# Kernel optimization log

Hardware: AMD Instinct MI355X
Metric: run time of the kernel (lower is better)

## Reference

```python
import jax, jax.numpy as jnp
import numpy as np

H = 1024      # hidden_size
I = 2 * H     # intermediate_size (expand_factor=2)
N = 16        # ssm_state_size
K = 4         # conv_kernel
BATCH = 2
SEQ = 2048


def setup_inputs() -> dict:
    key = jax.random.key(0)
    k = jax.random.split(key, 6)
    x = jax.random.normal(k[0], (BATCH, SEQ, H), dtype=jnp.float32)
    # nn.Linear default init ~ U(-1/sqrt(fan_in), 1/sqrt(fan_in)); scale is fine for a reference
    W_in = jax.random.normal(k[1], (2 * I, H), dtype=jnp.float32) / np.sqrt(H)
    conv_w = jax.random.normal(k[2], (I, 1, K), dtype=jnp.float32) / np.sqrt(K)
    W_x = jax.random.normal(k[3], (2 * N + 1, I), dtype=jnp.float32) / np.sqrt(I)
    A_log = jax.random.normal(k[4], (I, N), dtype=jnp.float32)
    D = jnp.ones((I,), dtype=jnp.float32)
    W_out = jax.random.normal(k[5], (H, I), dtype=jnp.float32) / np.sqrt(I)
    return {"x": x, "W_in": W_in, "conv_w": conv_w, "W_x": W_x,
            "A_log": A_log, "D": D, "W_out": W_out}


def reference(x, W_in, conv_w, W_x, A_log, D, W_out):
    xz = jnp.einsum('bsh,ih->bsi', x, W_in)
    xp, z = jnp.split(xz, 2, axis=-1)
    # depthwise causal conv1d: pad left K-1 (torch pads both sides then slices [:S])
    xc = jax.lax.conv_general_dilated(
        xp.transpose(0, 2, 1),           # (B, I, S)
        conv_w,                          # (I, 1, K) = OIH with groups=I
        window_strides=(1,),
        padding=[(K - 1, 0)],
        feature_group_count=I,
        dimension_numbers=('NCH', 'OIH', 'NCH'),
    ).transpose(0, 2, 1)                 # (B, S, I)
    xc = jax.nn.silu(xc)
    # x_proj -> delta (1), B (N), C (N)
    xproj = jnp.einsum('bsi,pi->bsp', xc, W_x)   # (B,S,2N+1)
    delta = jax.nn.softplus(xproj[..., :1])       # (B,S,1)
    Bmat = xproj[..., 1:1 + N]                    # (B,S,N)
    Cmat = xproj[..., 1 + N:]                     # (B,S,N)
    A = -jnp.exp(A_log)                           # (I,N)
    # decay/states broadcast-reduce: (B,S,I,N) intermediates reduced over N
    decay = jnp.exp(delta[..., None] * A[None, None])            # (B,S,I,N)
    states = xc[..., None] * Bmat[:, :, None, :] * decay          # (B,S,I,N)
    y = jnp.sum(states * Cmat[:, :, None, :], axis=-1)            # (B,S,I)
    y = y + xc * D[None, None, :]
    return jnp.einsum('bsi,hi->bsh', y * jax.nn.silu(z), W_out)
```

## Files before the change

### kernel.cpp

```cpp
#include <hip/hip_runtime.h>

#define LOG2E 1.4426950408889634f

__device__ __forceinline__ float b2f(unsigned short u) {
    unsigned int v = ((unsigned int)u) << 16;
    return __builtin_bit_cast(float, v);
}
__device__ __forceinline__ unsigned short f2b(float f) {
    unsigned int u = __builtin_bit_cast(unsigned int, f);
    u += 0x7fffu + ((u >> 16) & 1u);
    return (unsigned short)(u >> 16);
}
__device__ __forceinline__ float fexp(float x) {
    return __builtin_amdgcn_exp2f(x * LOG2E);
}
__device__ __forceinline__ float silu_f(float x) {
    return x * __builtin_amdgcn_rcpf(1.0f + fexp(-x));
}

typedef const __attribute__((address_space(1))) unsigned int* gas_t;
typedef __attribute__((address_space(3))) unsigned int* las_t;
__device__ __forceinline__ void gl2lds16(const unsigned short* g, unsigned short* l) {
    __builtin_amdgcn_global_load_lds((gas_t)(const void*)g, (las_t)(void*)l, 16, 0, 0);
}

__global__ __launch_bounds__(256) void cvt_all_k(const float* __restrict__ x,
                                                 const float* __restrict__ W_in,
                                                 const float* __restrict__ W_out,
                                                 const float* __restrict__ W_x,
                                                 unsigned short* __restrict__ xb,
                                                 unsigned short* __restrict__ wib,
                                                 unsigned short* __restrict__ wob,
                                                 unsigned short* __restrict__ wxb) {
    int b = blockIdx.x;
    const float* src;
    unsigned short* dst;
    if (b < 4096)       { src = x;     dst = xb;  }
    else if (b < 8192)  { src = W_in;  dst = wib; b -= 4096; }
    else if (b < 10240) { src = W_out; dst = wob; b -= 8192; }
    else                { src = W_x;   dst = wxb; b -= 10240; }
    int i = b * 256 + threadIdx.x;
    float4 v = ((const float4*)src)[i];
    *(ushort4*)(dst + (size_t)i * 4) = make_ushort4(f2b(v.x), f2b(v.y), f2b(v.z), f2b(v.w));
}

typedef __bf16 bf16x8 __attribute__((ext_vector_type(8)));
typedef float  fx4    __attribute__((ext_vector_type(4)));
typedef int    ix4    __attribute__((ext_vector_type(4)));
union FragU { ix4 i; bf16x8 b; };

template <bool OUT_BF16>
__global__ __launch_bounds__(256) void gemm_bt(const unsigned short* __restrict__ A,
                                               const unsigned short* __restrict__ B,
                                               void* __restrict__ C, int N, int K) {
    __shared__ __align__(16) unsigned short sA[128 * 64];
    __shared__ __align__(16) unsigned short sB[128 * 64];
    const int tid  = threadIdx.x;
    const int lane = tid & 63, wave = tid >> 6;
    const int bm = blockIdx.y * 128, bn = blockIdx.x * 128;
    const int wm = (wave >> 1) * 64, wn = (wave & 1) * 64;
    const int row16 = lane & 15, quad = lane >> 4;
    const int srow = lane >> 3;
    const int sc16 = (lane & 7) ^ srow;
    const unsigned short* gA = A + (size_t)(bm + wave * 32 + srow) * K + sc16 * 8;
    const unsigned short* gB = B + (size_t)(bn + wave * 32 + srow) * K + sc16 * 8;
    unsigned short* lA = sA + (wave * 4) * 512;
    unsigned short* lB = sB + (wave * 4) * 512;
    fx4 acc[4][4] = {};

    for (int kt = 0; kt < K; kt += 64) {
#pragma unroll
        for (int it = 0; it < 4; ++it) {
            gl2lds16(gA + (size_t)it * 8 * K + kt, lA + it * 512);
            gl2lds16(gB + (size_t)it * 8 * K + kt, lB + it * 512);
        }
        __syncthreads();
#pragma unroll
        for (int kk = 0; kk < 64; kk += 32) {
            FragU af[4], bf[4];
#pragma unroll
            for (int t = 0; t < 4; ++t) {
                int ra = wm + t * 16 + row16;
                af[t].i = *(const ix4*)(sA + ra * 64 + ((quad + (kk >> 3)) ^ (ra & 7)) * 8);
            }
#pragma unroll
            for (int t = 0; t < 4; ++t) {
                int rb = wn + t * 16 + row16;
                bf[t].i = *(const ix4*)(sB + rb * 64 + ((quad + (kk >> 3)) ^ (rb & 7)) * 8);
            }
#pragma unroll
            for (int tm = 0; tm < 4; ++tm)
#pragma unroll
                for (int tn = 0; tn < 4; ++tn)
                    acc[tm][tn] = __builtin_amdgcn_mfma_f32_16x16x32_bf16(
                        af[tm].b, bf[tn].b, acc[tm][tn], 0, 0, 0);
        }
        __syncthreads();
    }
#pragma unroll
    for (int tm = 0; tm < 4; ++tm) {
        int row0 = bm + wm + tm * 16 + quad * 4;
#pragma unroll
        for (int tn = 0; tn < 4; ++tn) {
            int col = bn + wn + tn * 16 + row16;
#pragma unroll
            for (int r = 0; r < 4; ++r) {
                float v = acc[tm][tn][r];
                if (OUT_BF16)
                    ((unsigned short*)C)[(size_t)(row0 + r) * N + col] = f2b(v);
                else
                    ((float*)C)[(size_t)(row0 + r) * N + col] = v;
            }
        }
    }
}

__global__ __launch_bounds__(256) void gemm_bt_n64(const unsigned short* __restrict__ A,
                                                   const unsigned short* __restrict__ B,
                                                   float* __restrict__ C, int N, int K) {
    __shared__ __align__(16) unsigned short sA[128 * 64];
    __shared__ __align__(16) unsigned short sB[64 * 64];
    const int tid  = threadIdx.x;
    const int lane = tid & 63, wave = tid >> 6;
    const int bm = blockIdx.y * 128, bn = blockIdx.x * 64;
    const int wm = wave * 32;
    const int row16 = lane & 15, quad = lane >> 4;
    const int srow = lane >> 3;
    const int sc16 = (lane & 7) ^ srow;
    const unsigned short* gA = A + (size_t)(bm + wave * 32 + srow) * K + sc16 * 8;
    const unsigned short* gB = B + (size_t)(bn + wave * 16 + srow) * K + sc16 * 8;
    unsigned short* lA = sA + (wave * 4) * 512;
    unsigned short* lB = sB + (wave * 2) * 512;
    fx4 acc[2][4] = {};

    for (int kt = 0; kt < K; kt += 64) {
#pragma unroll
        for (int it = 0; it < 4; ++it)
            gl2lds16(gA + (size_t)it * 8 * K + kt, lA + it * 512);
#pragma unroll
        for (int it = 0; it < 2; ++it)
            gl2lds16(gB + (size_t)it * 8 * K + kt, lB + it * 512);
        __syncthreads();
#pragma unroll
        for (int kk = 0; kk < 64; kk += 32) {
            FragU af[2], bf[4];
#pragma unroll
            for (int t = 0; t < 2; ++t) {
                int ra = wm + t * 16 + row16;
                af[t].i = *(const ix4*)(sA + ra * 64 + ((quad + (kk >> 3)) ^ (ra & 7)) * 8);
            }
#pragma unroll
            for (int t = 0; t < 4; ++t) {
                int rb = t * 16 + row16;
                bf[t].i = *(const ix4*)(sB + rb * 64 + ((quad + (kk >> 3)) ^ (rb & 7)) * 8);
            }
#pragma unroll
            for (int tm = 0; tm < 2; ++tm)
#pragma unroll
                for (int tn = 0; tn < 4; ++tn)
                    acc[tm][tn] = __builtin_amdgcn_mfma_f32_16x16x32_bf16(
                        af[tm].b, bf[tn].b, acc[tm][tn], 0, 0, 0);
        }
        __syncthreads();
    }
#pragma unroll
    for (int tm = 0; tm < 2; ++tm) {
        int row0 = bm + wm + tm * 16 + quad * 4;
#pragma unroll
        for (int tn = 0; tn < 4; ++tn) {
            int col = bn + tn * 16 + row16;
#pragma unroll
            for (int r = 0; r < 4; ++r)
                C[(size_t)(row0 + r) * N + col] = acc[tm][tn][r];
        }
    }
}

__global__ __launch_bounds__(256) void fused_mid_k(const unsigned short* __restrict__ xz,
                                                   const float* __restrict__ cw,
                                                   const unsigned short* __restrict__ wxb,
                                                   const float* __restrict__ Alog,
                                                   const float* __restrict__ Dv,
                                                   unsigned short* __restrict__ y2) {
    __shared__ __align__(16) unsigned short sxc[8 * 2048];
    __shared__ float sX[4][16][49];
    __shared__ float sdg[8 * 17];
    const int tid  = threadIdx.x;
    const int lane = tid & 63, wave = tid >> 6;
    const int row16 = lane & 15, quad = lane >> 4;
    const int m0 = blockIdx.x * 8;

    {
        const float4* cw4 = (const float4*)cw;
        float w[8][4];
#pragma unroll
        for (int c = 0; c < 8; ++c) {
            float4 t4 = cw4[tid * 8 + c];
            w[c][0] = t4.x; w[c][1] = t4.y; w[c][2] = t4.z; w[c][3] = t4.w;
        }
#pragma unroll
        for (int j = 0; j < 8; ++j) {
            const int m = m0 + j, s = m & 2047;
            float acc[8] = {0, 0, 0, 0, 0, 0, 0, 0};
#pragma unroll
            for (int k = 0; k < 4; ++k) {
                if (s - 3 + k >= 0) {
                    const unsigned short* p = xz + (size_t)(m - 3 + k) * 4096 + tid * 8;
                    ushort4 a = *(const ushort4*)p;
                    ushort4 b = *(const ushort4*)(p + 4);
                    float v[8] = {b2f(a.x), b2f(a.y), b2f(a.z), b2f(a.w),
                                  b2f(b.x), b2f(b.y), b2f(b.z), b2f(b.w)};
#pragma unroll
                    for (int c = 0; c < 8; ++c) acc[c] += v[c] * w[c][k];
                }
            }
            unsigned short* q = sxc + j * 2048 + ((tid ^ (j & 7)) * 8);
            *(ushort4*)q       = make_ushort4(f2b(silu_f(acc[0])), f2b(silu_f(acc[1])),
                                              f2b(silu_f(acc[2])), f2b(silu_f(acc[3])));
            *(ushort4*)(q + 4) = make_ushort4(f2b(silu_f(acc[4])), f2b(silu_f(acc[5])),
                                              f2b(silu_f(acc[6])), f2b(silu_f(acc[7])));
        }
    }
    __syncthreads();

    {
        fx4 acc[3] = {};
        const unsigned short* bp = wxb + (size_t)row16 * 2048 + wave * 512 + quad * 8;
        const int arow = row16 & 7;
        const int cbase = wave * 64 + quad;
#pragma unroll 4
        for (int kk = 0; kk < 512; kk += 32) {
            FragU a, b0, b1, b2;
            int c16 = cbase + (kk >> 3);
            a.i  = *(const ix4*)(sxc + arow * 2048 + ((c16 ^ (arow & 7)) * 8));
            b0.i = *(const ix4*)(bp + kk);
            b1.i = *(const ix4*)(bp + 16 * 2048 + kk);
            b2.i = *(const ix4*)(bp + 32 * 2048 + kk);
            acc[0] = __builtin_amdgcn_mfma_f32_16x16x32_bf16(a.b, b0.b, acc[0], 0, 0, 0);
            acc[1] = __builtin_amdgcn_mfma_f32_16x16x32_bf16(a.b, b1.b, acc[1], 0, 0, 0);
            acc[2] = __builtin_amdgcn_mfma_f32_16x16x32_bf16(a.b, b2.b, acc[2], 0, 0, 0);
        }
#pragma unroll
        for (int t = 0; t < 3; ++t)
#pragma unroll
            for (int r = 0; r < 4; ++r)
                sX[wave][quad * 4 + r][t * 16 + row16] = acc[t][r];
    }
    __syncthreads();
    for (int idx = tid; idx < 136; idx += 256) {
        int rr = idx / 17, q = idx - rr * 17;
        float o;
        if (q == 0) {
            float v = sX[0][rr][0] + sX[1][rr][0] + sX[2][rr][0] + sX[3][rr][0];
            o = (v > 20.f) ? v : log1pf(fexp(v));
        } else {
            float bs = sX[0][rr][q]      + sX[1][rr][q]      + sX[2][rr][q]      + sX[3][rr][q];
            float cs = sX[0][rr][q + 16] + sX[1][rr][q + 16] + sX[2][rr][q + 16] + sX[3][rr][q + 16];
            o = bs * cs;
        }
        sdg[rr * 17 + q] = o;
    }
    __syncthreads();

#pragma unroll 1
    for (int p = 0; p < 2; ++p) {
        const int ch0 = p * 1024 + tid * 4;
        float a2[4][16];
#pragma unroll
        for (int c = 0; c < 4; ++c) {
            const float4* ar = (const float4*)(Alog + (size_t)(ch0 + c) * 16);
#pragma unroll
            for (int n4 = 0; n4 < 4; ++n4) {
                float4 t4 = ar[n4];
                a2[c][n4 * 4 + 0] = -fexp(t4.x) * LOG2E;
                a2[c][n4 * 4 + 1] = -fexp(t4.y) * LOG2E;
                a2[c][n4 * 4 + 2] = -fexp(t4.z) * LOG2E;
                a2[c][n4 * 4 + 3] = -fexp(t4.w) * LOG2E;
            }
        }
        float4 dvv = *(const float4*)(Dv + ch0);
        float dv[4] = {dvv.x, dvv.y, dvv.z, dvv.w};
        const int c16 = ch0 >> 3, sub = ch0 & 7;
#pragma unroll 1
        for (int j = 0; j < 8; ++j) {
            const int m = m0 + j;
            float delta = sdg[j * 17];
            float Gr[16];
#pragma unroll
            for (int n = 0; n < 16; ++n) Gr[n] = sdg[j * 17 + 1 + n];
            ushort4 xu = *(const ushort4*)(sxc + j * 2048 + ((c16 ^ (j & 7)) * 8) + sub);
            ushort4 zu = *(const ushort4*)(xz + (size_t)m * 4096 + 2048 + ch0);
            float xcv[4] = {b2f(xu.x), b2f(xu.y), b2f(xu.z), b2f(xu.w)};
            float zv[4]  = {b2f(zu.x), b2f(zu.y), b2f(zu.z), b2f(zu.w)};
            unsigned short ov[4];
#pragma unroll
            for (int c = 0; c < 4; ++c) {
                float ssum = 0.f;
#pragma unroll
                for (int n = 0; n < 16; ++n)
                    ssum += Gr[n] * __builtin_amdgcn_exp2f(delta * a2[c][n]);
                float y = xcv[c] * (dv[c] + ssum);
                ov[c] = f2b(y * silu_f(zv[c]));
            }
            *(ushort4*)(y2 + (size_t)m * 2048 + ch0) = make_ushort4(ov[0], ov[1], ov[2], ov[3]);
        }
    }
}

extern "C" void kernel_launch(void* const* d_in, const int* in_sizes, int n_in,
                              void* d_out, int out_size, void* d_ws, size_t ws_size,
                              hipStream_t stream) {
    const float* x      = (const float*)d_in[0];
    const float* W_in   = (const float*)d_in[1];
    const float* conv_w = (const float*)d_in[2];
    const float* W_x    = (const float*)d_in[3];
    const float* A_log  = (const float*)d_in[4];
    const float* Dvec   = (const float*)d_in[5];
    const float* W_out  = (const float*)d_in[6];

    char* ws = (char*)d_ws;
    unsigned short* xb  = (unsigned short*)(ws);
    unsigned short* wib = (unsigned short*)(ws + 8388608);
    unsigned short* wob = (unsigned short*)(ws + 16777216);
    unsigned short* xz  = (unsigned short*)(ws + 20971520);
    unsigned short* y2  = (unsigned short*)(ws + 54525952);
    unsigned short* wxb = (unsigned short*)(ws + 71303168);

    cvt_all_k<<<10306, 256, 0, stream>>>(x, W_in, W_out, W_x, xb, wib, wob, wxb);
    gemm_bt<true><<<dim3(32, 32), 256, 0, stream>>>(xb, wib, xz, 4096, 1024);
    fused_mid_k<<<512, 256, 0, stream>>>(xz, conv_w, wxb, A_log, Dvec, y2);
    gemm_bt_n64<<<dim3(16, 32), 256, 0, stream>>>(y2, wob, (float*)d_out, 1024, 2048);
}
```

Before: 221.0 us.

## Split fused mid kernel into conv+xproj and conv+SSM kernels with precomputed A

Splits the fused middle kernel into two kernels. The first computes the conv, the x_proj MFMA and the delta/B*C terms, then writes them to a small global buffer. The second recomputes the depthwise conv per channel and performs the SSM reduction over a 2x512 grid, so twice as many blocks share the exp-heavy work. The -exp(A_log)*log2e precompute moves into the conversion kernel, and the conv loads now use a sliding window of 11 rows loaded once instead of per-tap reloads. The cost is an extra launch, a global round-trip for the dg values, and recomputing the conv.

```diff
diff --git a/kernel.cpp b/kernel.cpp
--- a/kernel.cpp
+++ b/kernel.cpp
@@ -17,6 +17,9 @@
 __device__ __forceinline__ float silu_f(float x) {
     return x * __builtin_amdgcn_rcpf(1.0f + fexp(-x));
 }
+__device__ __forceinline__ unsigned short u4get(ushort4 v, int c) {
+    return c == 0 ? v.x : c == 1 ? v.y : c == 2 ? v.z : v.w;
+}
 
 typedef const __attribute__((address_space(1))) unsigned int* gas_t;
 typedef __attribute__((address_space(3))) unsigned int* las_t;
@@ -28,11 +31,20 @@
                                                  const float* __restrict__ W_in,
                                                  const float* __restrict__ W_out,
                                                  const float* __restrict__ W_x,
+                                                 const float* __restrict__ Alog,
                                                  unsigned short* __restrict__ xb,
                                                  unsigned short* __restrict__ wib,
                                                  unsigned short* __restrict__ wob,
-                                                 unsigned short* __restrict__ wxb) {
+                                                 unsigned short* __restrict__ wxb,
+                                                 float* __restrict__ A2) {
     int b = blockIdx.x;
+    if (b >= 10306) {
+        int i = (b - 10306) * 256 + threadIdx.x;
+        float4 v = ((const float4*)Alog)[i];
+        ((float4*)A2)[i] = make_float4(-fexp(v.x) * LOG2E, -fexp(v.y) * LOG2E,
+                                       -fexp(v.z) * LOG2E, -fexp(v.w) * LOG2E);
+        return;
+    }
     const float* src;
     unsigned short* dst;
     if (b < 4096)       { src = x;     dst = xb;  }
@@ -176,43 +188,46 @@
     }
 }
 
-__global__ __launch_bounds__(256) void fused_mid_k(const unsigned short* __restrict__ xz,
-                                                   const float* __restrict__ cw,
-                                                   const unsigned short* __restrict__ wxb,
-                                                   const float* __restrict__ Alog,
-                                                   const float* __restrict__ Dv,
-                                                   unsigned short* __restrict__ y2) {
+__global__ __launch_bounds__(256) void conv_xproj_k(const unsigned short* __restrict__ xz,
+                                                    const float* __restrict__ cw,
+                                                    const unsigned short* __restrict__ wxb,
+                                                    float* __restrict__ dg) {
     __shared__ __align__(16) unsigned short sxc[8 * 2048];
     __shared__ float sX[4][16][49];
-    __shared__ float sdg[8 * 17];
     const int tid  = threadIdx.x;
     const int lane = tid & 63, wave = tid >> 6;
     const int row16 = lane & 15, quad = lane >> 4;
-    const int m0 = blockIdx.x * 8;
+    const int m0 = blockIdx.x * 8, s0 = m0 & 2047;
 
     {
+        ushort4 ua[11], ub[11];
+#pragma unroll
+        for (int t = 0; t < 11; ++t) {
+            int mr = (s0 - 3 + t >= 0) ? (m0 - 3 + t) : m0;
+            const unsigned short* p = xz + (size_t)mr * 4096 + tid * 8;
+            ua[t] = *(const ushort4*)p;
+            ub[t] = *(const ushort4*)(p + 4);
+        }
+        float w[8][4];
         const float4* cw4 = (const float4*)cw;
-        float w[8][4];
 #pragma unroll
         for (int c = 0; c < 8; ++c) {
             float4 t4 = cw4[tid * 8 + c];
             w[c][0] = t4.x; w[c][1] = t4.y; w[c][2] = t4.z; w[c][3] = t4.w;
         }
 #pragma unroll
+        for (int t = 0; t < 3; ++t)
+            if (s0 - 3 + t < 0) { ua[t] = make_ushort4(0, 0, 0, 0); ub[t] = make_ushort4(0, 0, 0, 0); }
+#pragma unroll
         for (int j = 0; j < 8; ++j) {
-            const int m = m0 + j, s = m & 2047;
             float acc[8] = {0, 0, 0, 0, 0, 0, 0, 0};
 #pragma unroll
             for (int k = 0; k < 4; ++k) {
-                if (s - 3 + k >= 0) {
-                    const unsigned short* p = xz + (size_t)(m - 3 + k) * 4096 + tid * 8;
-                    ushort4 a = *(const ushort4*)p;
-                    ushort4 b = *(const ushort4*)(p + 4);
-                    float v[8] = {b2f(a.x), b2f(a.y), b2f(a.z), b2f(a.w),
-                                  b2f(b.x), b2f(b.y), b2f(b.z), b2f(b.w)};
-#pragma unroll
-                    for (int c = 0; c < 8; ++c) acc[c] += v[c] * w[c][k];
-                }
+                ushort4 a = ua[j + k], b = ub[j + k];
+                float v[8] = {b2f(a.x), b2f(a.y), b2f(a.z), b2f(a.w),
+                              b2f(b.x), b2f(b.y), b2f(b.z), b2f(b.w)};
+#pragma unroll
+                for (int c = 0; c < 8; ++c) acc[c] += v[c] * w[c][k];
             }
             unsigned short* q = sxc + j * 2048 + ((tid ^ (j & 7)) * 8);
             *(ushort4*)q       = make_ushort4(f2b(silu_f(acc[0])), f2b(silu_f(acc[1])),
@@ -232,7 +247,7 @@
         for (int kk = 0; kk < 512; kk += 32) {
             FragU a, b0, b1, b2;
             int c16 = cbase + (kk >> 3);
-            a.i  = *(const ix4*)(sxc + arow * 2048 + ((c16 ^ (arow & 7)) * 8));
+            a.i  = *(const ix4*)(sxc + arow * 2048 + ((c16 ^ arow) * 8));
             b0.i = *(const ix4*)(bp + kk);
             b1.i = *(const ix4*)(bp + 16 * 2048 + kk);
             b2.i = *(const ix4*)(bp + 32 * 2048 + kk);
@@ -258,52 +273,79 @@
             float cs = sX[0][rr][q + 16] + sX[1][rr][q + 16] + sX[2][rr][q + 16] + sX[3][rr][q + 16];
             o = bs * cs;
         }
-        sdg[rr * 17 + q] = o;
-    }
+        dg[(size_t)(m0 + rr) * 17 + q] = o;
+    }
+}
+
+__global__ __launch_bounds__(256, 2) void conv_ssm_k(const unsigned short* __restrict__ xz,
+                                                     const float* __restrict__ cw,
+                                                     const float* __restrict__ dg,
+                                                     const float* __restrict__ A2,
+                                                     const float* __restrict__ Dv,
+                                                     unsigned short* __restrict__ y2) {
+    __shared__ float sdg[8 * 17];
+    const int tid = threadIdx.x;
+    const int m0 = blockIdx.y * 8, s0 = m0 & 2047;
+    const int ch0 = blockIdx.x * 1024 + tid * 4;
+    if (tid < 136) sdg[tid] = dg[(size_t)m0 * 17 + tid];
+
+    ushort4 uw[11];
+#pragma unroll
+    for (int t = 0; t < 11; ++t) {
+        int mr = (s0 - 3 + t >= 0) ? (m0 - 3 + t) : m0;
+        uw[t] = *(const ushort4*)(xz + (size_t)mr * 4096 + ch0);
+    }
+    ushort4 zu[8];
+#pragma unroll
+    for (int j = 0; j < 8; ++j)
+        zu[j] = *(const ushort4*)(xz + (size_t)(m0 + j) * 4096 + 2048 + ch0);
+    float w[4][4];
+    const float4* cw4 = (const float4*)cw;
+#pragma unroll
+    for (int c = 0; c < 4; ++c) {
+        float4 t4 = cw4[ch0 + c];
+        w[c][0] = t4.x; w[c][1] = t4.y; w[c][2] = t4.z; w[c][3] = t4.w;
+    }
+    float a2[4][16];
+#pragma unroll
+    for (int c = 0; c < 4; ++c) {
+        const float4* ar = (const float4*)(A2 + (size_t)(ch0 + c) * 16);
+#pragma unroll
+        for (int n4 = 0; n4 < 4; ++n4) {
+            float4 t4 = ar[n4];
+            a2[c][n4 * 4 + 0] = t4.x; a2[c][n4 * 4 + 1] = t4.y;
+            a2[c][n4 * 4 + 2] = t4.z; a2[c][n4 * 4 + 3] = t4.w;
+        }
+    }
+    float4 dvv = *(const float4*)(Dv + ch0);
+    float dv[4] = {dvv.x, dvv.y, dvv.z, dvv.w};
+#pragma unroll
+    for (int t = 0; t < 3; ++t)
+        if (s0 - 3 + t < 0) uw[t] = make_ushort4(0, 0, 0, 0);
     __syncthreads();
 
-#pragma unroll 1
-    for (int p = 0; p < 2; ++p) {
-        const int ch0 = p * 1024 + tid * 4;
-        float a2[4][16];
+#pragma unroll
+    for (int j = 0; j < 8; ++j) {
+        float delta = sdg[j * 17];
+        float Gr[16];
+#pragma unroll
+        for (int n = 0; n < 16; ++n) Gr[n] = sdg[j * 17 + 1 + n];
+        unsigned short ov[4];
 #pragma unroll
         for (int c = 0; c < 4; ++c) {
-            const float4* ar = (const float4*)(Alog + (size_t)(ch0 + c) * 16);
-#pragma unroll
-            for (int n4 = 0; n4 < 4; ++n4) {
-                float4 t4 = ar[n4];
-                a2[c][n4 * 4 + 0] = -fexp(t4.x) * LOG2E;
-                a2[c][n4 * 4 + 1] = -fexp(t4.y) * LOG2E;
-                a2[c][n4 * 4 + 2] = -fexp(t4.z) * LOG2E;
-                a2[c][n4 * 4 + 3] = -fexp(t4.w) * LOG2E;
-            }
-        }
-        float4 dvv = *(const float4*)(Dv + ch0);
-        float dv[4] = {dvv.x, dvv.y, dvv.z, dvv.w};
-        const int c16 = ch0 >> 3, sub = ch0 & 7;
-#pragma unroll 1
-        for (int j = 0; j < 8; ++j) {
-            const int m = m0 + j;
-            float delta = sdg[j * 17];
-            float Gr[16];
-#pragma unroll
-            for (int n = 0; n < 16; ++n) Gr[n] = sdg[j * 17 + 1 + n];
-            ushort4 xu = *(const ushort4*)(sxc + j * 2048 + ((c16 ^ (j & 7)) * 8) + sub);
-            ushort4 zu = *(const ushort4*)(xz + (size_t)m * 4096 + 2048 + ch0);
-            float xcv[4] = {b2f(xu.x), b2f(xu.y), b2f(xu.z), b2f(xu.w)};
-            float zv[4]  = {b2f(zu.x), b2f(zu.y), b2f(zu.z), b2f(zu.w)};
-            unsigned short ov[4];
-#pragma unroll
-            for (int c = 0; c < 4; ++c) {
-                float ssum = 0.f;
-#pragma unroll
-                for (int n = 0; n < 16; ++n)
-                    ssum += Gr[n] * __builtin_amdgcn_exp2f(delta * a2[c][n]);
-                float y = xcv[c] * (dv[c] + ssum);
-                ov[c] = f2b(y * silu_f(zv[c]));
-            }
-            *(ushort4*)(y2 + (size_t)m * 2048 + ch0) = make_ushort4(ov[0], ov[1], ov[2], ov[3]);
-        }
+            float acc = 0.f;
+#pragma unroll
+            for (int k = 0; k < 4; ++k)
+                acc += b2f(u4get(uw[j + k], c)) * w[c][k];
+            float xc = silu_f(acc);
+            float ssum = 0.f;
+#pragma unroll
+            for (int n = 0; n < 16; ++n)
+                ssum += Gr[n] * __builtin_amdgcn_exp2f(delta * a2[c][n]);
+            float y = xc * (dv[c] + ssum);
+            ov[c] = f2b(y * silu_f(b2f(u4get(zu[j], c))));
+        }
+        *(ushort4*)(y2 + (size_t)(m0 + j) * 2048 + ch0) = make_ushort4(ov[0], ov[1], ov[2], ov[3]);
     }
 }
 
@@ -325,9 +367,12 @@
     unsigned short* xz  = (unsigned short*)(ws + 20971520);
     unsigned short* y2  = (unsigned short*)(ws + 54525952);
     unsigned short* wxb = (unsigned short*)(ws + 71303168);
-
-    cvt_all_k<<<10306, 256, 0, stream>>>(x, W_in, W_out, W_x, xb, wib, wob, wxb);
+    float*          dgp = (float*)        (ws + 71499776);
+    float*          a2p = (float*)        (ws + 71778304);
+
+    cvt_all_k<<<10338, 256, 0, stream>>>(x, W_in, W_out, W_x, A_log, xb, wib, wob, wxb, a2p);
     gemm_bt<true><<<dim3(32, 32), 256, 0, stream>>>(xb, wib, xz, 4096, 1024);
-    fused_mid_k<<<512, 256, 0, stream>>>(xz, conv_w, wxb, A_log, Dvec, y2);
+    conv_xproj_k<<<512, 256, 0, stream>>>(xz, conv_w, wxb, dgp);
+    conv_ssm_k<<<dim3(2, 512), 256, 0, stream>>>(xz, conv_w, dgp, a2p, Dvec, y2);
     gemm_bt_n64<<<dim3(16, 32), 256, 0, stream>>>(y2, wob, (float*)d_out, 1024, 2048);
 }
```

Result: faster. 215.5 us (-2.5%).
